# Kernel optimization log

Hardware: AMD Instinct MI355X
Metric: run time of the kernel (lower is better)

Reference implementation:

```python
import jax, jax.numpy as jnp
import numpy as np

B, S, D = 4, 2048, 1024
LN_EPS = 1e-3  # keras LayerNormalization default


def setup_inputs() -> dict:
    key = jax.random.key(0)
    ks = jax.random.split(key, 4)
    std = 1.0 / np.sqrt(D)
    return {
        "inputs": jax.random.normal(ks[0], (B, S, D), dtype=jnp.float32),
        "Wq": jax.random.normal(ks[1], (D, D), dtype=jnp.float32) * std,
        "bq": jnp.zeros((D,), jnp.float32),
        "Wk": jax.random.normal(ks[2], (D, D), dtype=jnp.float32) * std,
        "bk": jnp.zeros((D,), jnp.float32),
        "Wv": jax.random.normal(ks[3], (D, D), dtype=jnp.float32) * std,
        "bv": jnp.zeros((D,), jnp.float32),
        "ln_gamma": jnp.ones((D,), jnp.float32),
        "ln_beta": jnp.zeros((D,), jnp.float32),
    }


def reference(inputs, Wq, bq, Wk, bk, Wv, bv, ln_gamma, ln_beta):
    d = inputs.shape[-1]
    scale = jnp.sqrt(jnp.asarray(d, inputs.dtype))
    q = inputs @ Wq + bq          # [B,S,D]
    k = inputs @ Wk + bk
    v = inputs @ Wv + bv
    scores = jnp.einsum("bqd,bkd->bqk", q, k) / scale  # [B,S,S]
    attn = jax.nn.softmax(scores, axis=-1)
    context = jnp.einsum("bqk,bkd->bqd", attn, v)      # [B,S,D]
    resid = context + inputs
    mu = jnp.mean(resid, axis=-1, keepdims=True)
    var = jnp.mean(jnp.square(resid - mu), axis=-1, keepdims=True)
    normed = (resid - mu) * jax.lax.rsqrt(var + LN_EPS)
    return normed * ln_gamma + ln_beta
```

## Files before the change

kernel.cpp:

```cpp
#include <hip/hip_runtime.h>
#include <hip/hip_bf16.h>
#include <cstdint>
#include <cstddef>


typedef unsigned short u16;
using bf16x8 = __attribute__((ext_vector_type(8))) short;
using f32x16 = __attribute__((ext_vector_type(16))) float;

typedef __attribute__((address_space(3))) unsigned int lds_uint;
typedef const __attribute__((address_space(1))) unsigned int glob_uint;

__device__ __forceinline__ float bf2f(u16 h) {
    union { unsigned int u; float f; } c;
    c.u = ((unsigned int)h) << 16;
    return c.f;
}
__device__ __forceinline__ u16 f2bf(float f) {
    union { float f; unsigned int u; } c;
    c.f = f;
    return (u16)((c.u + 0x7fffu + ((c.u >> 16) & 1u)) >> 16);
}
__device__ __forceinline__ void load_lds16(const void* g, void* l) {
    __builtin_amdgcn_global_load_lds((glob_uint*)g, (lds_uint*)l, 16, 0, 0);
}

__device__ __forceinline__ int detect_fp32(const u16* X, int* sflag) {
    const int t = threadIdx.x;
    if (t < 64) {
        bool bad = false, nz = false;
#pragma unroll
        for (int j = 0; j < 4; ++j) {
            float v = bf2f(X[(t * 4 + j) * 2]);
            if (!(fabsf(v) <= 1e9f)) bad = true;
            if (v != 0.f) nz = true;
        }
        unsigned long long ab = __ballot(bad);
        unsigned long long an = __ballot(nz);
        if (t == 0) *sflag = (ab != 0ull || an == 0ull) ? 1 : 0;
    }
    __syncthreads();
    return *sflag;
}

__global__ __launch_bounds__(256) void prep_kernel(
    const void* __restrict__ X, const void* __restrict__ Wq,
    const void* __restrict__ Wk, const void* __restrict__ Wv,
    const void* __restrict__ bq, const void* __restrict__ bk,
    const void* __restrict__ bv, const void* __restrict__ gamma,
    const void* __restrict__ beta,
    u16* __restrict__ Xb, u16* __restrict__ Wt, u16* __restrict__ bias5)
{
    __shared__ u16 tile[64][72];
    __shared__ int sflag;
    const int fp32 = detect_fp32((const u16*)X, &sflag);
    const int t   = threadIdx.x;
    const int blk = blockIdx.x;

    if (blk < 4096) {
        const size_t i = ((size_t)blk * 256 + t) * 8;
        if (fp32) {
            const float* f = (const float*)X;
            float4 a = *(const float4*)(f + i);
            float4 b = *(const float4*)(f + i + 4);
            ushort4 o0, o1;
            o0.x = f2bf(a.x); o0.y = f2bf(a.y); o0.z = f2bf(a.z); o0.w = f2bf(a.w);
            o1.x = f2bf(b.x); o1.y = f2bf(b.y); o1.z = f2bf(b.z); o1.w = f2bf(b.w);
            *(ushort4*)(Xb + i) = o0;
            *(ushort4*)(Xb + i + 4) = o1;
        } else {
            *(uint4*)(Xb + i) = *(const uint4*)((const u16*)X + i);
        }
    } else if (blk < 4864) {
        const int idx = blk - 4096;
        const int k0 = (idx & 15) * 64;
        const int n0 = ((idx >> 4) & 15) * 64;
        const int w  = idx >> 8;
        const void* W = (w == 0) ? Wq : ((w == 1) ? Wk : Wv);
#pragma unroll
        for (int it = 0; it < 2; ++it) {
            int i2 = t + it * 256;
            int r = i2 >> 3;
            int c = (i2 & 7) * 8;
            const size_t off = (size_t)(k0 + r) * 1024 + n0 + c;
            if (fp32) {
                const float* Wf = (const float*)W + off;
                float4 a = *(const float4*)Wf;
                float4 b = *(const float4*)(Wf + 4);
                u16* tp = &tile[r][c];
                tp[0] = f2bf(a.x); tp[1] = f2bf(a.y); tp[2] = f2bf(a.z); tp[3] = f2bf(a.w);
                tp[4] = f2bf(b.x); tp[5] = f2bf(b.y); tp[6] = f2bf(b.z); tp[7] = f2bf(b.w);
            } else {
                *(uint4*)&tile[r][c] = *(const uint4*)((const u16*)W + off);
            }
        }
        __syncthreads();
#pragma unroll
        for (int it = 0; it < 2; ++it) {
            int i2 = t + it * 256;
            int r = i2 >> 3;
            int c = (i2 & 7) * 8;
            union { u16 s[8]; uint4 v; } tmp;
#pragma unroll
            for (int j = 0; j < 8; ++j) tmp.s[j] = tile[c + j][r];
            *(uint4*)(Wt + (size_t)(w * 1024 + n0 + r) * 1024 + k0 + c) = tmp.v;
        }
    } else {
        const int v = blk - 4864;
        const void* srcs[5] = {bq, bk, bv, gamma, beta};
        const void* src = srcs[v];
        u16* d = bias5 + (size_t)v * 1024;
        const int i = t * 4;
        if (fp32) {
            const float* f = (const float*)src;
            ushort4 o;
            o.x = f2bf(f[i]); o.y = f2bf(f[i + 1]);
            o.z = f2bf(f[i + 2]); o.w = f2bf(f[i + 3]);
            *(ushort4*)(d + i) = o;
        } else {
            *(ushort4*)(d + i) = *(const ushort4*)((const u16*)src + i);
        }
    }
}

__global__ __launch_bounds__(256) void transpose_v4_kernel(
    const u16* __restrict__ QKV, u16* __restrict__ Vt4)
{
    __shared__ u16 tile[64][72];
    const int t  = threadIdx.x;
    const int k0 = blockIdx.x * 64;
    const int n0 = blockIdx.y * 64;
    const int b  = blockIdx.z;
    const u16* Vsrc = QKV + (size_t)b * 2048 * 3072 + 2048;
    u16* Vt = Vt4 + (size_t)b * 1024 * 2048;
#pragma unroll
    for (int it = 0; it < 2; ++it) {
        int idx = t + it * 256;
        int r = idx >> 3;
        int c = (idx & 7) * 8;
        *(uint4*)&tile[r][c] = *(const uint4*)(Vsrc + (size_t)(k0 + r) * 3072 + n0 + c);
    }
    __syncthreads();
#pragma unroll
    for (int it = 0; it < 2; ++it) {
        int idx = t + it * 256;
        int r = idx >> 3;
        int c = (idx & 7) * 8;
        union { u16 s[8]; uint4 v; } tmp;
#pragma unroll
        for (int j = 0; j < 8; ++j) tmp.s[j] = tile[c + j][r];
        *(uint4*)(Vt + (size_t)(n0 + r) * 2048 + k0 + c) = tmp.v;
    }
}

template<int EPI>
__global__ __launch_bounds__(256) void gemm128(
    const u16* __restrict__ A, int lda, size_t sA,
    const u16* __restrict__ Bt, int ldb, size_t sB,
    u16* __restrict__ C, int ldc, size_t sC,
    int K, float scale, const u16* __restrict__ bias3)
{
    __shared__ u16 As[2][128 * 32];
    __shared__ u16 Bs[2][128 * 32];
    const int t    = threadIdx.x;
    const int lane = t & 63;
    const int w    = t >> 6;
    const int wr   = w >> 1, wc = w & 1;
    const int m0 = blockIdx.y * 128;
    const int n0 = blockIdx.x * 128;
    A  += (size_t)blockIdx.z * sA;
    Bt += (size_t)blockIdx.z * sB;
    C  += (size_t)blockIdx.z * sC;

    const int srow = lane >> 2;
    const int skg  = (lane & 3) ^ ((srow >> 1) & 3);
    const u16* Ag0 = A  + (size_t)(m0 + w * 32 +      srow) * lda + skg * 8;
    const u16* Ag1 = A  + (size_t)(m0 + w * 32 + 16 + srow) * lda + skg * 8;
    const u16* Bg0 = Bt + (size_t)(n0 + w * 32 +      srow) * ldb + skg * 8;
    const u16* Bg1 = Bt + (size_t)(n0 + w * 32 + 16 + srow) * ldb + skg * 8;
    u16* Al0 = &As[0][(w * 32) * 32];
    u16* Al1 = &As[1][(w * 32) * 32];
    u16* Bl0 = &Bs[0][(w * 32) * 32];
    u16* Bl1 = &Bs[1][(w * 32) * 32];

    f32x16 acc[2][2];
#pragma unroll
    for (int mi = 0; mi < 2; ++mi)
#pragma unroll
        for (int ni = 0; ni < 2; ++ni)
#pragma unroll
            for (int r = 0; r < 16; ++r)
                acc[mi][ni][r] = 0.f;

    const int ml  = lane & 31;
    const int kh  = lane >> 5;
    const int key = (ml >> 1) & 3;

    for (int k0 = 0; k0 < K; k0 += 64) {
        load_lds16(Ag0 + k0,      Al0);
        load_lds16(Ag1 + k0,      Al0 + 16 * 32);
        load_lds16(Bg0 + k0,      Bl0);
        load_lds16(Bg1 + k0,      Bl0 + 16 * 32);
        load_lds16(Ag0 + k0 + 32, Al1);
        load_lds16(Ag1 + k0 + 32, Al1 + 16 * 32);
        load_lds16(Bg0 + k0 + 32, Bl1);
        load_lds16(Bg1 + k0 + 32, Bl1 + 16 * 32);
        __syncthreads();
#pragma unroll
        for (int slab = 0; slab < 2; ++slab) {
            const u16* as_ = As[slab];
            const u16* bs_ = Bs[slab];
#pragma unroll
            for (int s = 0; s < 2; ++s) {
                const int g    = s * 2 + kh;
                const int slot = (g ^ key) * 8;
                bf16x8 a0 = *(const bf16x8*)&as_[(wr * 64 +      ml) * 32 + slot];
                bf16x8 a1 = *(const bf16x8*)&as_[(wr * 64 + 32 + ml) * 32 + slot];
                bf16x8 b0 = *(const bf16x8*)&bs_[(wc * 64 +      ml) * 32 + slot];
                bf16x8 b1 = *(const bf16x8*)&bs_[(wc * 64 + 32 + ml) * 32 + slot];
                acc[0][0] = __builtin_amdgcn_mfma_f32_32x32x16_bf16(a0, b0, acc[0][0], 0, 0, 0);
                acc[0][1] = __builtin_amdgcn_mfma_f32_32x32x16_bf16(a0, b1, acc[0][1], 0, 0, 0);
                acc[1][0] = __builtin_amdgcn_mfma_f32_32x32x16_bf16(a1, b0, acc[1][0], 0, 0, 0);
                acc[1][1] = __builtin_amdgcn_mfma_f32_32x32x16_bf16(a1, b1, acc[1][1], 0, 0, 0);
            }
        }
        __syncthreads();
    }

    const int colb = n0 + wc * 64 + ml;
    const int rowb = m0 + wr * 64 + 4 * kh;
#pragma unroll
    for (int mi = 0; mi < 2; ++mi) {
#pragma unroll
        for (int ni = 0; ni < 2; ++ni) {
            const int col = colb + ni * 32;
            const float bias = (EPI == 0) ? bf2f(bias3[col]) : 0.f;
#pragma unroll
            for (int r = 0; r < 16; ++r) {
                const int row = rowb + mi * 32 + (r & 3) + 8 * (r >> 2);
                C[(size_t)row * ldc + col] = f2bf(acc[mi][ni][r] * scale + bias);
            }
        }
    }
}

__global__ __launch_bounds__(256) void softmax_bf16_kernel(u16* __restrict__ S)
{
    const int t = threadIdx.x;
    u16* sp = S + (size_t)blockIdx.x * 2048;
    union { uint4 v; u16 h[8]; } raw;
    raw.v = *(const uint4*)(sp + t * 8);
    float vals[8];
#pragma unroll
    for (int i = 0; i < 8; ++i) vals[i] = bf2f(raw.h[i]);
    float m = vals[0];
#pragma unroll
    for (int i = 1; i < 8; ++i) m = fmaxf(m, vals[i]);
#pragma unroll
    for (int off = 32; off > 0; off >>= 1) m = fmaxf(m, __shfl_xor(m, off));
    __shared__ float red[8];
    const int w = t >> 6, lane = t & 63;
    if (lane == 0) red[w] = m;
    __syncthreads();
    m = fmaxf(fmaxf(red[0], red[1]), fmaxf(red[2], red[3]));
    float e[8], s = 0.f;
#pragma unroll
    for (int i = 0; i < 8; ++i) { e[i] = __expf(vals[i] - m); s += e[i]; }
#pragma unroll
    for (int off = 32; off > 0; off >>= 1) s += __shfl_xor(s, off);
    if (lane == 0) red[4 + w] = s;
    __syncthreads();
    s = red[4] + red[5] + red[6] + red[7];
    const float rinv = 1.f / s;
    union { uint4 v; u16 h[8]; } out;
#pragma unroll
    for (int i = 0; i < 8; ++i) out.h[i] = f2bf(e[i] * rinv);
    *(uint4*)(sp + t * 8) = out.v;
}

__global__ __launch_bounds__(256) void resid_ln_kernel(
    const u16* __restrict__ Ctx, const u16* __restrict__ Xb,
    const u16* __restrict__ gamma, const u16* __restrict__ beta,
    void* __restrict__ Out, const u16* __restrict__ Xraw)
{
    __shared__ int sflag;
    const int fp32 = detect_fp32(Xraw, &sflag);
    const size_t row = blockIdx.x;
    const int t = threadIdx.x;
    ushort4 cv = *(const ushort4*)(Ctx + row * 3072 + t * 4);
    ushort4 xv = *(const ushort4*)(Xb + row * 1024 + t * 4);
    float v[4] = {bf2f(cv.x) + bf2f(xv.x), bf2f(cv.y) + bf2f(xv.y),
                  bf2f(cv.z) + bf2f(xv.z), bf2f(cv.w) + bf2f(xv.w)};
    float s  = v[0] + v[1] + v[2] + v[3];
    float s2 = v[0] * v[0] + v[1] * v[1] + v[2] * v[2] + v[3] * v[3];
#pragma unroll
    for (int off = 32; off > 0; off >>= 1) {
        s  += __shfl_xor(s, off);
        s2 += __shfl_xor(s2, off);
    }
    __shared__ float red[8];
    const int w = t >> 6, lane = t & 63;
    if (lane == 0) { red[w] = s; red[4 + w] = s2; }
    __syncthreads();
    s  = red[0] + red[1] + red[2] + red[3];
    s2 = red[4] + red[5] + red[6] + red[7];
    const float mu  = s * (1.f / 1024.f);
    const float var = s2 * (1.f / 1024.f) - mu * mu;
    const float inv = rsqrtf(var + 1e-3f);
    ushort4 gv = *(const ushort4*)(gamma + t * 4);
    ushort4 bv = *(const ushort4*)(beta + t * 4);
    float o[4];
    o[0] = (v[0] - mu) * inv * bf2f(gv.x) + bf2f(bv.x);
    o[1] = (v[1] - mu) * inv * bf2f(gv.y) + bf2f(bv.y);
    o[2] = (v[2] - mu) * inv * bf2f(gv.z) + bf2f(bv.z);
    o[3] = (v[3] - mu) * inv * bf2f(gv.w) + bf2f(bv.w);
    if (fp32) {
        float4 fo = {o[0], o[1], o[2], o[3]};
        *(float4*)((float*)Out + row * 1024 + t * 4) = fo;
    } else {
        ushort4 bo;
        bo.x = f2bf(o[0]); bo.y = f2bf(o[1]); bo.z = f2bf(o[2]); bo.w = f2bf(o[3]);
        *(ushort4*)((u16*)Out + row * 1024 + t * 4) = bo;
    }
}

extern "C" void kernel_launch(void* const* d_in, const int* in_sizes, int n_in,
                              void* d_out, int out_size, void* d_ws, size_t ws_size,
                              hipStream_t stream)
{
    (void)in_sizes; (void)n_in; (void)out_size; (void)ws_size;
    const void* X     = d_in[0];
    const void* Wq    = d_in[1];
    const void* bq    = d_in[2];
    const void* Wk    = d_in[3];
    const void* bk    = d_in[4];
    const void* Wv    = d_in[5];
    const void* bv    = d_in[6];
    const void* gamma = d_in[7];
    const void* beta  = d_in[8];

    char* ws = (char*)d_ws;
    u16* bias5 = (u16*)(ws + 16);
    u16* Wt    = (u16*)(ws + 16384);
    u16* QKV   = (u16*)(ws + 6307840);
    u16* Xb    = (u16*)(ws + 56639488);
    u16* S4    = (u16*)(ws + 73416704);
    u16* Vt4   = (u16*)(ws + 106971136);

    prep_kernel<<<4869, 256, 0, stream>>>(
        X, Wq, Wk, Wv, bq, bk, bv, gamma, beta, Xb, Wt, bias5);

    gemm128<0><<<dim3(24, 64, 1), 256, 0, stream>>>(
        Xb, 1024, 0, Wt, 1024, 0, QKV, 3072, 0, 1024, 1.f, bias5);

    gemm128<1><<<dim3(16, 16, 4), 256, 0, stream>>>(
        QKV, 3072, (size_t)2048 * 3072,
        QKV + 1024, 3072, (size_t)2048 * 3072,
        S4, 2048, (size_t)2048 * 2048, 1024, 0.03125f, nullptr);

    softmax_bf16_kernel<<<8192, 256, 0, stream>>>(S4);

    transpose_v4_kernel<<<dim3(32, 16, 4), 256, 0, stream>>>(QKV, Vt4);

    gemm128<1><<<dim3(8, 16, 4), 256, 0, stream>>>(
        S4, 2048, (size_t)2048 * 2048,
        Vt4, 2048, (size_t)1024 * 2048,
        QKV, 3072, (size_t)2048 * 3072, 2048, 1.f, nullptr);

    resid_ln_kernel<<<8192, 256, 0, stream>>>(
        QKV, Xb, bias5 + 3 * 1024, bias5 + 4 * 1024, d_out, (const u16*)X);
}
```

Before: 299.0 us.

## Replace 128x128 GEMM with 256-row tiles and 4-stage async LDS pipeline

Replaces the 128x128, 256-thread GEMM with a 512-thread kernel using 256xBN tiles (BN 128 or 256). Global-to-LDS loads now run through a 4-slot ring with prefetch three stages ahead, gated by explicit vmcnt waits and raw s_barrier, instead of load-then-sync every iteration. It also raises wave priority around the MFMA block. This aims at better data reuse per tile and hiding load latency behind MFMA work, at the cost of more LDS per block, higher register pressure and fewer blocks for the smaller GEMMs.

```diff
diff --git a/kernel.cpp b/kernel.cpp
--- a/kernel.cpp
+++ b/kernel.cpp
@@ -153,84 +153,116 @@
     }
 }
 
-template<int EPI>
-__global__ __launch_bounds__(256) void gemm128(
+template<int EPI, int BN>
+__global__ __launch_bounds__(512, 2) void gemm256(
     const u16* __restrict__ A, int lda, size_t sA,
     const u16* __restrict__ Bt, int ldb, size_t sB,
     u16* __restrict__ C, int ldc, size_t sC,
     int K, float scale, const u16* __restrict__ bias3)
 {
-    __shared__ u16 As[2][128 * 32];
-    __shared__ u16 Bs[2][128 * 32];
-    const int t    = threadIdx.x;
-    const int lane = t & 63;
-    const int w    = t >> 6;
-    const int wr   = w >> 1, wc = w & 1;
-    const int m0 = blockIdx.y * 128;
-    const int n0 = blockIdx.x * 128;
+    constexpr int WAVES_M = (BN == 256) ? 2 : 4;
+    constexpr int WM = 256 / WAVES_M;
+    constexpr int MF = WM / 32;
+    __shared__ u16 As[4][256 * 32];
+    __shared__ u16 Bs[4][BN * 32];
+
+    const int t  = threadIdx.x;
+    const int l  = t & 63;
+    const int w  = t >> 6;
+    const int wm = (BN == 256) ? (w >> 2) : (w >> 1);
+    const int wn = (BN == 256) ? (w & 3)  : (w & 1);
+    const int m0 = blockIdx.y * 256;
+    const int n0 = blockIdx.x * BN;
     A  += (size_t)blockIdx.z * sA;
     Bt += (size_t)blockIdx.z * sB;
     C  += (size_t)blockIdx.z * sC;
 
-    const int srow = lane >> 2;
-    const int skg  = (lane & 3) ^ ((srow >> 1) & 3);
-    const u16* Ag0 = A  + (size_t)(m0 + w * 32 +      srow) * lda + skg * 8;
-    const u16* Ag1 = A  + (size_t)(m0 + w * 32 + 16 + srow) * lda + skg * 8;
-    const u16* Bg0 = Bt + (size_t)(n0 + w * 32 +      srow) * ldb + skg * 8;
-    const u16* Bg1 = Bt + (size_t)(n0 + w * 32 + 16 + srow) * ldb + skg * 8;
-    u16* Al0 = &As[0][(w * 32) * 32];
-    u16* Al1 = &As[1][(w * 32) * 32];
-    u16* Bl0 = &Bs[0][(w * 32) * 32];
-    u16* Bl1 = &Bs[1][(w * 32) * 32];
-
-    f32x16 acc[2][2];
-#pragma unroll
-    for (int mi = 0; mi < 2; ++mi)
+    const int sa = (t & 3) ^ ((t >> 3) & 3);
+    const u16* Ag0 = A  + (size_t)(m0 + (t >> 2)) * lda + sa * 8;
+    const u16* Ag1 = Ag0 + (size_t)128 * lda;
+    const u16* Bg0 = Bt + (size_t)(n0 + (t >> 2)) * ldb + sa * 8;
+    const u16* Bg1 = Bg0 + (size_t)128 * ldb;
+
+    const int lr   = l & 31;
+    const int key  = (lr >> 1) & 3;
+    const int sp0  = (l >> 5) ^ key;
+    const int aoff = (wm * WM + lr) * 32;
+    const int boff = (wn * 64 + lr) * 32;
+
+    f32x16 acc[MF][2];
+#pragma unroll
+    for (int mi = 0; mi < MF; ++mi)
 #pragma unroll
         for (int ni = 0; ni < 2; ++ni)
 #pragma unroll
-            for (int r = 0; r < 16; ++r)
-                acc[mi][ni][r] = 0.f;
-
-    const int ml  = lane & 31;
-    const int kh  = lane >> 5;
-    const int key = (ml >> 1) & 3;
-
-    for (int k0 = 0; k0 < K; k0 += 64) {
-        load_lds16(Ag0 + k0,      Al0);
-        load_lds16(Ag1 + k0,      Al0 + 16 * 32);
-        load_lds16(Bg0 + k0,      Bl0);
-        load_lds16(Bg1 + k0,      Bl0 + 16 * 32);
-        load_lds16(Ag0 + k0 + 32, Al1);
-        load_lds16(Ag1 + k0 + 32, Al1 + 16 * 32);
-        load_lds16(Bg0 + k0 + 32, Bl1);
-        load_lds16(Bg1 + k0 + 32, Bl1 + 16 * 32);
-        __syncthreads();
-#pragma unroll
-        for (int slab = 0; slab < 2; ++slab) {
-            const u16* as_ = As[slab];
-            const u16* bs_ = Bs[slab];
-#pragma unroll
-            for (int s = 0; s < 2; ++s) {
-                const int g    = s * 2 + kh;
-                const int slot = (g ^ key) * 8;
-                bf16x8 a0 = *(const bf16x8*)&as_[(wr * 64 +      ml) * 32 + slot];
-                bf16x8 a1 = *(const bf16x8*)&as_[(wr * 64 + 32 + ml) * 32 + slot];
-                bf16x8 b0 = *(const bf16x8*)&bs_[(wc * 64 +      ml) * 32 + slot];
-                bf16x8 b1 = *(const bf16x8*)&bs_[(wc * 64 + 32 + ml) * 32 + slot];
-                acc[0][0] = __builtin_amdgcn_mfma_f32_32x32x16_bf16(a0, b0, acc[0][0], 0, 0, 0);
-                acc[0][1] = __builtin_amdgcn_mfma_f32_32x32x16_bf16(a0, b1, acc[0][1], 0, 0, 0);
-                acc[1][0] = __builtin_amdgcn_mfma_f32_32x32x16_bf16(a1, b0, acc[1][0], 0, 0, 0);
-                acc[1][1] = __builtin_amdgcn_mfma_f32_32x32x16_bf16(a1, b1, acc[1][1], 0, 0, 0);
-            }
-        }
-        __syncthreads();
-    }
-
-    const int colb = n0 + wc * 64 + ml;
-    const int rowb = m0 + wr * 64 + 4 * kh;
-#pragma unroll
-    for (int mi = 0; mi < 2; ++mi) {
+            for (int r = 0; r < 16; ++r) acc[mi][ni][r] = 0.f;
+
+    const int NS = K >> 5;
+
+    auto stage = [&](int j, int sl) {
+        const size_t ko = (size_t)j * 32;
+        load_lds16(Ag0 + ko, &As[sl][w * 512]);
+        load_lds16(Ag1 + ko, &As[sl][4096 + w * 512]);
+        load_lds16(Bg0 + ko, &Bs[sl][w * 512]);
+        if constexpr (BN == 256) load_lds16(Bg1 + ko, &Bs[sl][4096 + w * 512]);
+    };
+
+    stage(0, 0); stage(1, 1); stage(2, 2);
+    if constexpr (BN == 256) asm volatile("s_waitcnt vmcnt(8)" ::: "memory");
+    else                     asm volatile("s_waitcnt vmcnt(6)" ::: "memory");
+    __builtin_amdgcn_s_barrier();
+    asm volatile("" ::: "memory");
+
+    for (int j = 0; j < NS; ++j) {
+        const int sl = j & 3;
+        bf16x8 a[MF][2], b[2][2];
+        const u16* as_ = &As[sl][aoff];
+        const u16* bs_ = &Bs[sl][boff];
+#pragma unroll
+        for (int ks = 0; ks < 2; ++ks) {
+            const int sp = (ks ? (sp0 ^ 2) : sp0) * 8;
+#pragma unroll
+            for (int mi = 0; mi < MF; ++mi)
+                a[mi][ks] = *(const bf16x8*)(as_ + mi * 1024 + sp);
+#pragma unroll
+            for (int ni = 0; ni < 2; ++ni)
+                b[ni][ks] = *(const bf16x8*)(bs_ + ni * 1024 + sp);
+        }
+        if (j + 3 < NS) stage(j + 3, (j + 3) & 3);
+        const int rem = NS - 2 - j;
+        if (rem >= 2) {
+            if constexpr (BN == 256) asm volatile("s_waitcnt vmcnt(8)" ::: "memory");
+            else                     asm volatile("s_waitcnt vmcnt(6)" ::: "memory");
+        } else if (rem == 1) {
+            if constexpr (BN == 256) asm volatile("s_waitcnt vmcnt(4)" ::: "memory");
+            else                     asm volatile("s_waitcnt vmcnt(3)" ::: "memory");
+        } else if (rem == 0) {
+            asm volatile("s_waitcnt vmcnt(0)" ::: "memory");
+        }
+        if (j + 1 < NS) {
+            __builtin_amdgcn_s_barrier();
+            asm volatile("" ::: "memory");
+        }
+        __builtin_amdgcn_s_setprio(1);
+#pragma unroll
+        for (int ks = 0; ks < 2; ++ks)
+#pragma unroll
+            for (int mi = 0; mi < MF; ++mi)
+#pragma unroll
+                for (int ni = 0; ni < 2; ++ni)
+                    acc[mi][ni] = __builtin_amdgcn_mfma_f32_32x32x16_bf16(
+                        a[mi][ks], b[ni][ks], acc[mi][ni], 0, 0, 0);
+        __builtin_amdgcn_s_setprio(0);
+        if (j + 1 < NS) {
+            __builtin_amdgcn_s_barrier();
+            asm volatile("" ::: "memory");
+        }
+    }
+
+    const int colb = n0 + wn * 64 + lr;
+    const int rowb = m0 + wm * WM + 4 * (l >> 5);
+#pragma unroll
+    for (int mi = 0; mi < MF; ++mi) {
 #pragma unroll
         for (int ni = 0; ni < 2; ++ni) {
             const int col = colb + ni * 32;
@@ -350,10 +382,10 @@
     prep_kernel<<<4869, 256, 0, stream>>>(
         X, Wq, Wk, Wv, bq, bk, bv, gamma, beta, Xb, Wt, bias5);
 
-    gemm128<0><<<dim3(24, 64, 1), 256, 0, stream>>>(
+    gemm256<0, 128><<<dim3(24, 32, 1), 512, 0, stream>>>(
         Xb, 1024, 0, Wt, 1024, 0, QKV, 3072, 0, 1024, 1.f, bias5);
 
-    gemm128<1><<<dim3(16, 16, 4), 256, 0, stream>>>(
+    gemm256<1, 256><<<dim3(8, 8, 4), 512, 0, stream>>>(
         QKV, 3072, (size_t)2048 * 3072,
         QKV + 1024, 3072, (size_t)2048 * 3072,
         S4, 2048, (size_t)2048 * 2048, 1024, 0.03125f, nullptr);
@@ -362,7 +394,7 @@
 
     transpose_v4_kernel<<<dim3(32, 16, 4), 256, 0, stream>>>(QKV, Vt4);
 
-    gemm128<1><<<dim3(8, 16, 4), 256, 0, stream>>>(
+    gemm256<1, 128><<<dim3(8, 8, 4), 512, 0, stream>>>(
         S4, 2048, (size_t)2048 * 2048,
         Vt4, 2048, (size_t)1024 * 2048,
         QKV, 3072, (size_t)2048 * 3072, 2048, 1.f, nullptr);
```

After: 298.5 us. About the same (-0.2%).
